# Kernel tuning notes

Hardware: AMD Instinct MI355X
Metric: run time of the kernel (lower is better)

## Reference

```python
import jax, jax.numpy as jnp
import numpy as np

N_NODES = 50000
N_EDGES = 800000
N_GRAPHS = 256
F_IN = 32
HEADS = 8
NEG_SLOPE = 0.2


def gat_conv(x, W, a_src, a_dst, bias, src, dst, n_nodes, heads, ch):
    # x: [N, Fin], W: [Fin, heads*ch], a_src/a_dst: [heads, ch], bias: [heads*ch]
    h = (x @ W).reshape(n_nodes, heads, ch)              # [N,H,C]
    alpha_src = jnp.sum(h * a_src, axis=-1)              # [N,H]
    alpha_dst = jnp.sum(h * a_dst, axis=-1)              # [N,H]
    logit = alpha_src[src] + alpha_dst[dst]              # [E,H]
    logit = jax.nn.leaky_relu(logit, NEG_SLOPE)
    # segment softmax over edges grouped by destination node
    m = jax.ops.segment_max(logit, dst, num_segments=n_nodes)   # [N,H]
    m = jnp.where(jnp.isfinite(m), m, 0.0)
    e = jnp.exp(logit - m[dst])                          # [E,H]
    denom = jax.ops.segment_sum(e, dst, num_segments=n_nodes)   # [N,H]
    alpha = e / (denom[dst] + 1e-16)                     # [E,H]
    msg = h[src] * alpha[:, :, None]                     # [E,H,C]
    out = jax.ops.segment_sum(msg, dst, num_segments=n_nodes)   # [N,H,C]
    return out.reshape(n_nodes, heads * ch) + bias


def setup_inputs() -> dict:
    key = jax.random.key(0)
    ks = jax.random.split(key, 20)
    H = HEADS
    glorot = lambda k, shape: jax.random.normal(k, shape, jnp.float32) * (2.0 / (shape[0] + shape[-1])) ** 0.5
    inp = {
        "x": jax.random.normal(ks[0], (N_NODES, F_IN), jnp.float32),
        "W1": glorot(ks[1], (F_IN, H * 8)),
        "a_src1": glorot(ks[2], (H, 8)),
        "a_dst1": glorot(ks[3], (H, 8)),
        "b1": jnp.zeros((H * 8,), jnp.float32),
        "W2": glorot(ks[4], (64, H * 16)),
        "a_src2": glorot(ks[5], (H, 16)),
        "a_dst2": glorot(ks[6], (H, 16)),
        "b2": jnp.zeros((H * 16,), jnp.float32),
        "W3": glorot(ks[7], (128, H * 16)),
        "a_src3": glorot(ks[8], (H, 16)),
        "a_dst3": glorot(ks[9], (H, 16)),
        "b3": jnp.zeros((H * 16,), jnp.float32),
        "fc1_w": glorot(ks[10], (128, 10)),
        "fc1_b": jnp.zeros((10,), jnp.float32),
        "fc2_w": glorot(ks[11], (10, 1)),
        "fc2_b": jnp.zeros((1,), jnp.float32),
        "edge_index": jax.random.randint(ks[12], (2, N_EDGES), 0, N_NODES, jnp.int64 if jax.config.jax_enable_x64 else jnp.int32),
        "batch_vec": jnp.sort(jax.random.randint(ks[13], (N_NODES,), 0, N_GRAPHS, jnp.int32)),
        "num_graphs": N_GRAPHS,
    }
    return inp


def reference(x, W1, a_src1, a_dst1, b1, W2, a_src2, a_dst2, b2,
              W3, a_src3, a_dst3, b3, fc1_w, fc1_b, fc2_w, fc2_b,
              edge_index, batch_vec, num_graphs):
    n = x.shape[0]
    loops = jnp.arange(n, dtype=edge_index.dtype)
    src = jnp.concatenate([edge_index[0], loops])  # PyG GATConv add_self_loops=True
    dst = jnp.concatenate([edge_index[1], loops])

    h = jax.nn.elu(gat_conv(x, W1, a_src1, a_dst1, b1, src, dst, n, HEADS, 8))
    h = jax.nn.elu(gat_conv(h, W2, a_src2, a_dst2, b2, src, dst, n, HEADS, 16))
    h = jax.nn.elu(gat_conv(h, W3, a_src3, a_dst3, b3, src, dst, n, HEADS, 16))

    # global mean pool over graphs
    sums = jax.ops.segment_sum(h, batch_vec, num_segments=num_graphs)
    counts = jax.ops.segment_sum(jnp.ones((n,), h.dtype), batch_vec, num_segments=num_graphs)
    pooled = sums / jnp.maximum(counts, 1.0)[:, None]   # [G,128]

    z = jax.nn.relu(pooled @ fc1_w + fc1_b)
    return z @ fc2_w + fc2_b                             # [G,1]
```

## Files before the change

kernel.cpp:

```cpp
#include <hip/hip_runtime.h>
#include <hip/hip_bf16.h>

#define N_NODES   50000
#define N_EDGES   800000
#define N_TOT     850000
#define N_GRAPHS  256
#define HEADS     8
#define NEG_SLOPE 0.2f

template<int FIN, int FOUT>
__global__ __launch_bounds__(256) void gemm_kernel(const float* __restrict__ X,
                                                   const float* __restrict__ W,
                                                   float* __restrict__ H,
                                                   const float* __restrict__ a_src,
                                                   const float* __restrict__ a_dst,
                                                   float* __restrict__ asrc_o,
                                                   float* __restrict__ adst_o) {
    constexpr int KC    = 32;
    constexpr int THR_F = FOUT / 4;
    constexpr int NPT   = 64 / (256 / THR_F);
    constexpr int XS_S  = 68;
    constexpr int CH    = FOUT / 8;
    __shared__ float xs[KC * XS_S];
    __shared__ float ws[KC * FOUT];
    const int t = threadIdx.x;
    const int node0 = blockIdx.x * 64;
    const int fo  = (t % THR_F) * 4;
    const int ndb = (t / THR_F) * NPT;
    float4 acc[NPT];
#pragma unroll
    for (int i = 0; i < NPT; ++i) acc[i] = make_float4(0.f, 0.f, 0.f, 0.f);

    const int xn = t >> 2, ks = (t & 3) * 8;
    for (int kc = 0; kc < FIN; kc += KC) {
        __syncthreads();
        float4 a0 = make_float4(0.f,0.f,0.f,0.f), a1 = a0;
        if (node0 + xn < N_NODES) {
            const float* xp = X + (size_t)(node0 + xn) * FIN + kc + ks;
            a0 = *(const float4*)xp;
            a1 = *(const float4*)(xp + 4);
        }
        xs[(ks + 0) * XS_S + xn] = a0.x;
        xs[(ks + 1) * XS_S + xn] = a0.y;
        xs[(ks + 2) * XS_S + xn] = a0.z;
        xs[(ks + 3) * XS_S + xn] = a0.w;
        xs[(ks + 4) * XS_S + xn] = a1.x;
        xs[(ks + 5) * XS_S + xn] = a1.y;
        xs[(ks + 6) * XS_S + xn] = a1.z;
        xs[(ks + 7) * XS_S + xn] = a1.w;
        constexpr int WF4 = KC * FOUT / 4 / 256;
        const float4* wsrc = (const float4*)(W + (size_t)kc * FOUT);
        float4* wdst = (float4*)ws;
#pragma unroll
        for (int i = 0; i < WF4; ++i) wdst[t * WF4 + i] = wsrc[t * WF4 + i];
        __syncthreads();
#pragma unroll 4
        for (int k = 0; k < KC; ++k) {
            float4 wv = *(const float4*)(ws + k * FOUT + fo);
#pragma unroll
            for (int q = 0; q < NPT / 4; ++q) {
                float4 xv = *(const float4*)(xs + k * XS_S + ndb + q * 4);
                acc[q*4+0].x += xv.x * wv.x; acc[q*4+0].y += xv.x * wv.y;
                acc[q*4+0].z += xv.x * wv.z; acc[q*4+0].w += xv.x * wv.w;
                acc[q*4+1].x += xv.y * wv.x; acc[q*4+1].y += xv.y * wv.y;
                acc[q*4+1].z += xv.y * wv.z; acc[q*4+1].w += xv.y * wv.w;
                acc[q*4+2].x += xv.z * wv.x; acc[q*4+2].y += xv.z * wv.y;
                acc[q*4+2].z += xv.z * wv.z; acc[q*4+2].w += xv.z * wv.w;
                acc[q*4+3].x += xv.w * wv.x; acc[q*4+3].y += xv.w * wv.y;
                acc[q*4+3].z += xv.w * wv.z; acc[q*4+3].w += xv.w * wv.w;
            }
        }
    }
    const int h   = fo / CH;
    const float4 asv = *(const float4*)(a_src + h * CH + (fo % CH));
    const float4 adv = *(const float4*)(a_dst + h * CH + (fo % CH));
    constexpr int LPH = CH / 4;
#pragma unroll
    for (int i = 0; i < NPT; ++i) {
        int row = node0 + ndb + i;
        if (row < N_NODES) *(float4*)(H + (size_t)row * FOUT + fo) = acc[i];
        float s = acc[i].x*asv.x + acc[i].y*asv.y + acc[i].z*asv.z + acc[i].w*asv.w;
        float d = acc[i].x*adv.x + acc[i].y*adv.y + acc[i].z*adv.z + acc[i].w*adv.w;
        s += __shfl_xor(s, 1, 64);
        d += __shfl_xor(d, 1, 64);
        if (LPH == 4) { s += __shfl_xor(s, 2, 64); d += __shfl_xor(d, 2, 64); }
        if ((t & (LPH - 1)) == 0 && row < N_NODES) {
            asrc_o[row * 8 + h] = s;
            adst_o[row * 8 + h] = d;
        }
    }
}

__global__ void hist_kernel(const int* __restrict__ edst, int* __restrict__ cnt) {
    int e = blockIdx.x * blockDim.x + threadIdx.x;
    if (e >= N_TOT) return;
    int d = (e < N_EDGES) ? edst[e] : e - N_EDGES;
    atomicAdd(&cnt[d], 1);
}

__global__ void scan1_kernel(const int* __restrict__ cnt, int* __restrict__ excl,
                             int* __restrict__ bsum) {
    __shared__ int sm[256];
    int t = threadIdx.x;
    int i = blockIdx.x * 256 + t;
    int v = (i < N_NODES) ? cnt[i] : 0;
    sm[t] = v;
    __syncthreads();
    for (int off = 1; off < 256; off <<= 1) {
        int x = (t >= off) ? sm[t - off] : 0;
        __syncthreads();
        sm[t] += x;
        __syncthreads();
    }
    if (i < N_NODES) excl[i] = sm[t] - v;
    if (t == 255) bsum[blockIdx.x] = sm[255];
}

__global__ void scan2_kernel(int* __restrict__ bsum, int nblk) {
    __shared__ int sm[256];
    int t = threadIdx.x;
    int v = (t < nblk) ? bsum[t] : 0;
    sm[t] = v;
    __syncthreads();
    for (int off = 1; off < 256; off <<= 1) {
        int x = (t >= off) ? sm[t - off] : 0;
        __syncthreads();
        sm[t] += x;
        __syncthreads();
    }
    if (t < nblk) bsum[t] = sm[t] - v;
}

__global__ void scan3_kernel(const int* __restrict__ excl, const int* __restrict__ bsum,
                             int* __restrict__ row_ptr) {
    int i = blockIdx.x * blockDim.x + threadIdx.x;
    if (i < N_NODES) row_ptr[i] = excl[i] + bsum[i >> 8];
    if (i == N_NODES) row_ptr[N_NODES] = N_TOT;
}

__global__ void scatter_kernel(const int* __restrict__ esrc, const int* __restrict__ edst,
                               const int* __restrict__ row_ptr, int* __restrict__ cursor,
                               int* __restrict__ edge_src) {
    int e = blockIdx.x * blockDim.x + threadIdx.x;
    if (e >= N_TOT) return;
    int s, d;
    if (e < N_EDGES) { s = esrc[e]; d = edst[e]; } else { s = d = e - N_EDGES; }
    int pos = row_ptr[d] + atomicAdd(&cursor[d], 1);
    edge_src[pos] = s;
}

template<int CH>
__global__ __launch_bounds__(256) void gat_gather_kernel(
        const int* __restrict__ row_ptr, const int* __restrict__ edge_src,
        const float* __restrict__ asrc, const float* __restrict__ adst,
        const float* __restrict__ H, const float* __restrict__ bias,
        float* __restrict__ out) {
    constexpr int LPE   = 2 * CH;
    constexpr int SPLIT = 64 / LPE;
    constexpr int LPH   = CH / 4;
    constexpr int HS    = 8 * CH;
    const int n = (blockIdx.x * blockDim.x + threadIdx.x) >> 6;
    if (n >= N_NODES) return;
    const int lane = threadIdx.x & 63;
    const int sub = lane / LPE;
    const int li  = lane & (LPE - 1);
    const int h   = li / LPH;
    const int off = h * CH + (li & (LPH - 1)) * 4;
    const float adst_h = adst[n * 8 + h];
    const int e0 = row_ptr[n], e1 = row_ptr[n + 1];
    float sum = 0.f;
    float4 acc = make_float4(0.f, 0.f, 0.f, 0.f);
    int e = e0 + sub;
    for (; e + 3 * SPLIT < e1; e += 4 * SPLIT) {
        int s0 = edge_src[e];
        int s1 = edge_src[e + SPLIT];
        int s2 = edge_src[e + 2 * SPLIT];
        int s3 = edge_src[e + 3 * SPLIT];
        float l0 = asrc[s0 * 8 + h] + adst_h;
        float l1 = asrc[s1 * 8 + h] + adst_h;
        float l2 = asrc[s2 * 8 + h] + adst_h;
        float l3 = asrc[s3 * 8 + h] + adst_h;
        float4 h0 = *(const float4*)(H + (size_t)s0 * HS + off);
        float4 h1 = *(const float4*)(H + (size_t)s1 * HS + off);
        float4 h2 = *(const float4*)(H + (size_t)s2 * HS + off);
        float4 h3 = *(const float4*)(H + (size_t)s3 * HS + off);
        l0 = l0 > 0.f ? l0 : NEG_SLOPE * l0;
        l1 = l1 > 0.f ? l1 : NEG_SLOPE * l1;
        l2 = l2 > 0.f ? l2 : NEG_SLOPE * l2;
        l3 = l3 > 0.f ? l3 : NEG_SLOPE * l3;
        float w0 = __expf(l0), w1 = __expf(l1), w2 = __expf(l2), w3 = __expf(l3);
        sum += (w0 + w1) + (w2 + w3);
        acc.x += w0 * h0.x + w1 * h1.x + w2 * h2.x + w3 * h3.x;
        acc.y += w0 * h0.y + w1 * h1.y + w2 * h2.y + w3 * h3.y;
        acc.z += w0 * h0.z + w1 * h1.z + w2 * h2.z + w3 * h3.z;
        acc.w += w0 * h0.w + w1 * h1.w + w2 * h2.w + w3 * h3.w;
    }
    for (; e < e1; e += SPLIT) {
        int s = edge_src[e];
        float l = asrc[s * 8 + h] + adst_h;
        float4 hv = *(const float4*)(H + (size_t)s * HS + off);
        l = l > 0.f ? l : NEG_SLOPE * l;
        float w = __expf(l);
        sum += w;
        acc.x += w * hv.x;
        acc.y += w * hv.y;
        acc.z += w * hv.z;
        acc.w += w * hv.w;
    }
#pragma unroll
    for (int mask = LPE; mask < 64; mask <<= 1) {
        sum   += __shfl_xor(sum, mask, 64);
        acc.x += __shfl_xor(acc.x, mask, 64);
        acc.y += __shfl_xor(acc.y, mask, 64);
        acc.z += __shfl_xor(acc.z, mask, 64);
        acc.w += __shfl_xor(acc.w, mask, 64);
    }
    float inv = 1.0f / (sum + 1e-16f);
    float4 bv = *(const float4*)(bias + off);
    float4 v;
    v.x = acc.x * inv + bv.x;  v.x = v.x > 0.f ? v.x : expm1f(v.x);
    v.y = acc.y * inv + bv.y;  v.y = v.y > 0.f ? v.y : expm1f(v.y);
    v.z = acc.z * inv + bv.z;  v.z = v.z > 0.f ? v.z : expm1f(v.z);
    v.w = acc.w * inv + bv.w;  v.w = v.w > 0.f ? v.w : expm1f(v.w);
    *(float4*)(out + (size_t)n * HS + off) = v;
}

__global__ void gstart_kernel(const int* __restrict__ batch, int* __restrict__ gstart) {
    int g = threadIdx.x;
    int lo = 0, hi = N_NODES;
    while (lo < hi) {
        int mid = (lo + hi) >> 1;
        if (batch[mid] < g) lo = mid + 1; else hi = mid;
    }
    gstart[g] = lo;
    if (g == 0) gstart[N_GRAPHS] = N_NODES;
}

__global__ __launch_bounds__(512) void pool_head_kernel(
        const float* __restrict__ act, const int* __restrict__ gstart,
        const float* __restrict__ fc1_w, const float* __restrict__ fc1_b,
        const float* __restrict__ fc2_w, const float* __restrict__ fc2_b,
        float* __restrict__ out) {
    int g = blockIdx.x;
    int t = threadIdx.x;
    int f = t & 127, strip = t >> 7;
    int n0 = gstart[g], n1 = gstart[g + 1];
    float s = 0.f;
    for (int n = n0 + strip; n < n1; n += 4) s += act[(size_t)n * 128 + f];
    __shared__ float sm[4][128];
    __shared__ float zz[10];
    sm[strip][f] = s;
    __syncthreads();
    if (strip == 0) {
        float cnt = (float)(n1 - n0);
        cnt = cnt > 1.f ? cnt : 1.f;
        sm[0][f] = (sm[0][f] + sm[1][f] + sm[2][f] + sm[3][f]) / cnt;
    }
    __syncthreads();
    if (t < 10) {
        float z = fc1_b[t];
        for (int q = 0; q < 128; ++q) z += sm[0][q] * fc1_w[q * 10 + t];
        zz[t] = z > 0.f ? z : 0.f;
    }
    __syncthreads();
    if (t == 0) {
        float o = fc2_b[0];
#pragma unroll
        for (int j = 0; j < 10; ++j) o += zz[j] * fc2_w[j];
        out[g] = o;
    }
}

extern "C" void kernel_launch(void* const* d_in, const int* in_sizes, int n_in,
                              void* d_out, int out_size, void* d_ws, size_t ws_size,
                              hipStream_t stream) {
    const float* x      = (const float*)d_in[0];
    const float* W1     = (const float*)d_in[1];
    const float* a_src1 = (const float*)d_in[2];
    const float* a_dst1 = (const float*)d_in[3];
    const float* b1     = (const float*)d_in[4];
    const float* W2     = (const float*)d_in[5];
    const float* a_src2 = (const float*)d_in[6];
    const float* a_dst2 = (const float*)d_in[7];
    const float* b2     = (const float*)d_in[8];
    const float* W3     = (const float*)d_in[9];
    const float* a_src3 = (const float*)d_in[10];
    const float* a_dst3 = (const float*)d_in[11];
    const float* b3     = (const float*)d_in[12];
    const float* fc1_w  = (const float*)d_in[13];
    const float* fc1_b  = (const float*)d_in[14];
    const float* fc2_w  = (const float*)d_in[15];
    const float* fc2_b  = (const float*)d_in[16];
    const int*   eidx   = (const int*)d_in[17];
    const int*   batch  = (const int*)d_in[18];
    const int* esrc = eidx;
    const int* edst = eidx + N_EDGES;
    float* out = (float*)d_out;

    float* ws      = (float*)d_ws;
    float* h_buf   = ws;
    float* act0    = h_buf + 6400000;
    float* act1    = act0 + 6400000;
    float* asrcb   = act1 + 6400000;
    float* adstb   = asrcb + 400000;
    int*   cnt     = (int*)(adstb + 400000);
    int*   cursor  = cnt + 50000;
    int*   excl    = cursor + 50000;
    int*   bsum    = excl + 50000;
    int*   row_ptr = bsum + 256;
    int*   edge_src= row_ptr + 50001;
    int*   gstart  = edge_src + 850000;

    const int B = 256;
    dim3 blk(B);
    dim3 g_gemm((N_NODES + 63) / 64);
    dim3 g_edge((N_TOT + B - 1) / B);
    dim3 g_gather((N_NODES * 64 + B - 1) / B);
    const int nblk_scan = (N_NODES + 255) / 256;

    hipMemsetAsync(cnt, 0, 100000 * 4, stream);
    hist_kernel<<<g_edge, blk, 0, stream>>>(edst, cnt);
    scan1_kernel<<<dim3(nblk_scan), blk, 0, stream>>>(cnt, excl, bsum);
    scan2_kernel<<<dim3(1), blk, 0, stream>>>(bsum, nblk_scan);
    scan3_kernel<<<dim3((N_NODES + B) / B), blk, 0, stream>>>(excl, bsum, row_ptr);
    scatter_kernel<<<g_edge, blk, 0, stream>>>(esrc, edst, row_ptr, cursor, edge_src);
    gstart_kernel<<<dim3(1), blk, 0, stream>>>(batch, gstart);

    gemm_kernel<32, 64><<<g_gemm, blk, 0, stream>>>(x, W1, h_buf, a_src1, a_dst1,
                                                    asrcb, adstb);
    gat_gather_kernel<8><<<g_gather, blk, 0, stream>>>(row_ptr, edge_src, asrcb, adstb,
                                                       h_buf, b1, act0);

    gemm_kernel<64, 128><<<g_gemm, blk, 0, stream>>>(act0, W2, h_buf, a_src2, a_dst2,
                                                     asrcb, adstb);
    gat_gather_kernel<16><<<g_gather, blk, 0, stream>>>(row_ptr, edge_src, asrcb, adstb,
                                                        h_buf, b2, act1);

    gemm_kernel<128, 128><<<g_gemm, blk, 0, stream>>>(act1, W3, h_buf, a_src3, a_dst3,
                                                      asrcb, adstb);
    gat_gather_kernel<16><<<g_gather, blk, 0, stream>>>(row_ptr, edge_src, asrcb, adstb,
                                                        h_buf, b3, act0);

    pool_head_kernel<<<dim3(N_GRAPHS), dim3(512), 0, stream>>>(act0, gstart, fc1_w, fc1_b,
                                                               fc2_w, fc2_b, out);
}
```

Measured before the change: 349.1 us.

## Merge CSR scan kernels into one single-block scan and vectorize edge hist/scatter

```diff
diff --git a/kernel.cpp b/kernel.cpp
--- a/kernel.cpp
+++ b/kernel.cpp
@@ -92,61 +92,74 @@
 }
 
 __global__ void hist_kernel(const int* __restrict__ edst, int* __restrict__ cnt) {
-    int e = blockIdx.x * blockDim.x + threadIdx.x;
-    if (e >= N_TOT) return;
-    int d = (e < N_EDGES) ? edst[e] : e - N_EDGES;
-    atomicAdd(&cnt[d], 1);
-}
-
-__global__ void scan1_kernel(const int* __restrict__ cnt, int* __restrict__ excl,
-                             int* __restrict__ bsum) {
-    __shared__ int sm[256];
-    int t = threadIdx.x;
-    int i = blockIdx.x * 256 + t;
-    int v = (i < N_NODES) ? cnt[i] : 0;
-    sm[t] = v;
+    int i = blockIdx.x * blockDim.x + threadIdx.x;
+    if (i >= N_EDGES / 4) return;
+    int4 d4 = ((const int4*)edst)[i];
+    atomicAdd(&cnt[d4.x], 1);
+    atomicAdd(&cnt[d4.y], 1);
+    atomicAdd(&cnt[d4.z], 1);
+    atomicAdd(&cnt[d4.w], 1);
+}
+
+__global__ __launch_bounds__(1024) void scan_kernel(const int* __restrict__ cnt,
+                                                    int* __restrict__ row_ptr,
+                                                    const int* __restrict__ batch,
+                                                    int* __restrict__ gstart) {
+    constexpr int EPT = 49;
+    __shared__ int sm[1024];
+    const int t = threadIdx.x;
+    if (t < N_GRAPHS) {
+        int lo = 0, hi = N_NODES;
+        while (lo < hi) {
+            int mid = (lo + hi) >> 1;
+            if (batch[mid] < t) lo = mid + 1; else hi = mid;
+        }
+        gstart[t] = lo;
+        if (t == 0) gstart[N_GRAPHS] = N_NODES;
+    }
+    int base = t * EPT;
+    int local[EPT];
+    int s = 0;
+#pragma unroll
+    for (int i = 0; i < EPT; ++i) {
+        int idx = base + i;
+        int v = (idx < N_NODES) ? (cnt[idx] + 1) : 0;
+        local[i] = s;
+        s += v;
+    }
+    sm[t] = s;
     __syncthreads();
-    for (int off = 1; off < 256; off <<= 1) {
+    for (int off = 1; off < 1024; off <<= 1) {
         int x = (t >= off) ? sm[t - off] : 0;
         __syncthreads();
         sm[t] += x;
         __syncthreads();
     }
-    if (i < N_NODES) excl[i] = sm[t] - v;
-    if (t == 255) bsum[blockIdx.x] = sm[255];
-}
-
-__global__ void scan2_kernel(int* __restrict__ bsum, int nblk) {
-    __shared__ int sm[256];
-    int t = threadIdx.x;
-    int v = (t < nblk) ? bsum[t] : 0;
-    sm[t] = v;
-    __syncthreads();
-    for (int off = 1; off < 256; off <<= 1) {
-        int x = (t >= off) ? sm[t - off] : 0;
-        __syncthreads();
-        sm[t] += x;
-        __syncthreads();
-    }
-    if (t < nblk) bsum[t] = sm[t] - v;
-}
-
-__global__ void scan3_kernel(const int* __restrict__ excl, const int* __restrict__ bsum,
-                             int* __restrict__ row_ptr) {
-    int i = blockIdx.x * blockDim.x + threadIdx.x;
-    if (i < N_NODES) row_ptr[i] = excl[i] + bsum[i >> 8];
-    if (i == N_NODES) row_ptr[N_NODES] = N_TOT;
+    int tbase = sm[t] - s;
+#pragma unroll
+    for (int i = 0; i < EPT; ++i) {
+        int idx = base + i;
+        if (idx < N_NODES) row_ptr[idx] = tbase + local[i];
+    }
+    if (t == 1023) row_ptr[N_NODES] = N_TOT;
 }
 
 __global__ void scatter_kernel(const int* __restrict__ esrc, const int* __restrict__ edst,
                                const int* __restrict__ row_ptr, int* __restrict__ cursor,
                                int* __restrict__ edge_src) {
-    int e = blockIdx.x * blockDim.x + threadIdx.x;
-    if (e >= N_TOT) return;
-    int s, d;
-    if (e < N_EDGES) { s = esrc[e]; d = edst[e]; } else { s = d = e - N_EDGES; }
-    int pos = row_ptr[d] + atomicAdd(&cursor[d], 1);
-    edge_src[pos] = s;
+    int i = blockIdx.x * blockDim.x + threadIdx.x;
+    if (i < N_EDGES / 4) {
+        int4 s4 = ((const int4*)esrc)[i];
+        int4 d4 = ((const int4*)edst)[i];
+        int p;
+        p = row_ptr[d4.x] + 1 + atomicAdd(&cursor[d4.x], 1); edge_src[p] = s4.x;
+        p = row_ptr[d4.y] + 1 + atomicAdd(&cursor[d4.y], 1); edge_src[p] = s4.y;
+        p = row_ptr[d4.z] + 1 + atomicAdd(&cursor[d4.z], 1); edge_src[p] = s4.z;
+        p = row_ptr[d4.w] + 1 + atomicAdd(&cursor[d4.w], 1); edge_src[p] = s4.w;
+    } else if (i < N_EDGES / 4 + N_NODES) {
+        int d = i - N_EDGES / 4;
+        edge_src[row_ptr[d]] = d;
+    }
 }
 
 template<int CH>
@@ -225,17 +238,6 @@
     *(float4*)(out + (size_t)n * HS + off) = v;
 }
 
-__global__ void gstart_kernel(const int* __restrict__ batch, int* __restrict__ gstart) {
-    int g = threadIdx.x;
-    int lo = 0, hi = N_NODES;
-    while (lo < hi) {
-        int mid = (lo + hi) >> 1;
-        if (batch[mid] < g) lo = mid + 1; else hi = mid;
-    }
-    gstart[g] = lo;
-    if (g == 0) gstart[N_GRAPHS] = N_NODES;
-}
-
 __global__ __launch_bounds__(512) void pool_head_kernel(
         const float* __restrict__ act, const int* __restrict__ gstart,
         const float* __restrict__ fc1_w, const float* __restrict__ fc1_b,
@@ -305,26 +307,21 @@
     float* adstb   = asrcb + 400000;
     int*   cnt     = (int*)(adstb + 400000);
     int*   cursor  = cnt + 50000;
-    int*   excl    = cursor + 50000;
-    int*   bsum    = excl + 50000;
-    int*   row_ptr = bsum + 256;
+    int*   row_ptr = cursor + 50000;
     int*   edge_src= row_ptr + 50001;
     int*   gstart  = edge_src + 850000;
 
     const int B = 256;
     dim3 blk(B);
     dim3 g_gemm((N_NODES + 63) / 64);
-    dim3 g_edge((N_TOT + B - 1) / B);
+    dim3 g_hist((N_EDGES / 4 + B - 1) / B);
+    dim3 g_scat((N_EDGES / 4 + N_NODES + B - 1) / B);
     dim3 g_gather((N_NODES * 64 + B - 1) / B);
-    const int nblk_scan = (N_NODES + 255) / 256;
 
     hipMemsetAsync(cnt, 0, 100000 * 4, stream);
-    hist_kernel<<<g_edge, blk, 0, stream>>>(edst, cnt);
-    scan1_kernel<<<dim3(nblk_scan), blk, 0, stream>>>(cnt, excl, bsum);
-    scan2_kernel<<<dim3(1), blk, 0, stream>>>(bsum, nblk_scan);
-    scan3_kernel<<<dim3((N_NODES + B) / B), blk, 0, stream>>>(excl, bsum, row_ptr);
-    scatter_kernel<<<g_edge, blk, 0, stream>>>(esrc, edst, row_ptr, cursor, edge_src);
-    gstart_kernel<<<dim3(1), blk, 0, stream>>>(batch, gstart);
+    hist_kernel<<<g_hist, blk, 0, stream>>>(edst, cnt);
+    scan_kernel<<<dim3(1), dim3(1024), 0, stream>>>(cnt, row_ptr, batch, gstart);
+    scatter_kernel<<<g_scat, blk, 0, stream>>>(esrc, edst, row_ptr, cursor, edge_src);
 
     gemm_kernel<32, 64><<<g_gemm, blk, 0, stream>>>(x, W1, h_buf, a_src1, a_dst1,
                                                     asrcb, adstb);
```

After: 403.1 us. 1.15x slower.
